# Optimization experiments

Measured on AMD Instinct MI355X. Metric: run time of the kernel, lower is better.

Reference implementation:

```python
import jax, jax.numpy as jnp
import numpy as np

NUM_FEATURE = 50


def setup_inputs() -> dict:
    key = jax.random.key(0)
    k1, k2 = jax.random.split(key)
    query = jax.random.normal(k1, (512, NUM_FEATURE), dtype=jnp.float32)
    doc = jax.random.normal(k2, (512, 256, NUM_FEATURE), dtype=jnp.float32)
    # nn.Linear(150, 1, bias=False) with weight filled with 1
    W = jnp.ones((3 * NUM_FEATURE,), dtype=jnp.float32)
    return {"query": query, "doc": doc, "W": W}


def reference(query, doc, W):
    # Split the single 150-dim linear weight into the three trilinear parts:
    # score(x, y) = w1.sen_x + w2.q_y + w3.(sen_x * q_y)
    w1, w2, w3 = W[:NUM_FEATURE], W[NUM_FEATURE:2 * NUM_FEATURE], W[2 * NUM_FEATURE:]
    q_term = query @ w2                      # [Lq]
    qw3 = query * w3                         # [Lq, d]

    def per_sentence(sen):                   # sen: [Ls, d]
        sXY = (sen @ w1)[:, None] + q_term[None, :] + sen @ qw3.T   # [Ls, Lq]
        sD2Q = jax.nn.softmax(sXY, axis=0)   # softmax over sentence tokens
        sQ2D = jax.nn.softmax(sXY, axis=1)   # softmax over query tokens
        aD2Q = sD2Q @ query                  # [Ls, d]
        aQ2D = sD2Q @ (sQ2D.T @ sen)         # (sD2Q @ sQ2D.T) @ sen, cheaper order
        return jnp.concatenate([sen, aD2Q, sen * aD2Q, sen * aQ2D], axis=1)  # [Ls, 4d]

    return jax.vmap(per_sentence)(doc)       # [n_sen, Ls, 4d]
```

## Files before the change

### kernel.cpp

```cpp
#include <hip/hip_runtime.h>
#include <math.h>

typedef __bf16 bf16_t;
typedef bf16_t bf16x2 __attribute__((ext_vector_type(2)));
typedef bf16_t bf16x4 __attribute__((ext_vector_type(4)));
typedef bf16_t bf16x8 __attribute__((ext_vector_type(8)));
typedef float f32x4 __attribute__((ext_vector_type(4)));

#define MFMA16(a,b,c) __builtin_amdgcn_mfma_f32_16x16x32_bf16((a),(b),(c),0,0,0)

#define ND 256
#define NQ 512
#define NF 50
#define L2E 1.44269504f
#define SHIFT 64.0f

#define SENT_E 0
#define PQ_E   16896
#define PD_E   33792
#define QW3_E  52224
#define QTT_E  61440
#define GT_E   70656
#define PART_B  150528
#define STATS_B 154624
#define LDS_BYTES 157952

#define ST_QTERM 0
#define ST_CI    512
#define ST_RINV  576

__launch_bounds__(1024, 4)
__global__ void ca12_kernel(const float* __restrict__ query,
                            const float* __restrict__ doc,
                            const float* __restrict__ W,
                            float* __restrict__ out)
{
    extern __shared__ char smem[];
    bf16_t* lb = (bf16_t*)smem;
    float* part  = (float*)(smem + PART_B);
    float* stats = (float*)(smem + STATS_B);

    const int tid = threadIdx.x;
    const int w = tid >> 6, l = tid & 63, ln = l & 15, lg = l >> 4;
    const int s = blockIdx.x;
    const float* sen_g = doc + (size_t)s * (ND * NF);

    auto stageQW3 = [&](int jt, int buf, int tbase, int tn) {
        const int j0 = jt * 64;
        bf16_t* dst = lb + QW3_E + buf * 4608;
        for (int e = tid - tbase; e < 1664; e += tn) {
            int jj = e / 26, c = e - jj * 26;
            if (c < 25) {
                float2 v = ((const float2*)query)[(j0 + jj) * 25 + c];
                bf16x2 p;
                p[0] = (bf16_t)(v.x * W[100 + 2 * c] * L2E);
                p[1] = (bf16_t)(v.y * W[100 + 2 * c + 1] * L2E);
                *(bf16x2*)&dst[jj * 72 + 2 * c] = p;
            } else {
                bf16x2 p;
                p[0] = (bf16_t)(stats[ST_QTERM + j0 + jj] * L2E);
                p[1] = (bf16_t)L2E;
                *(bf16x2*)&dst[jj * 72 + 50] = p;
            }
        }
    };
    auto stageQTT = [&](int jt, int buf, int tbase, int tn) {
        const int j0 = jt * 64;
        bf16_t* dst = lb + QTT_E + buf * 4608;
        for (int e = tid - tbase; e < 1600; e += tn) {
            int c = e >> 6, jj = e & 63;
            float2 v = ((const float2*)query)[(j0 + jj) * 25 + c];
            dst[(2 * c) * 72 + jj]     = (bf16_t)v.x;
            dst[(2 * c + 1) * 72 + jj] = (bf16_t)v.y;
        }
    };

    for (int e = tid; e < 924; e += 1024) {
        int f = 50 + e / 66, c4 = (e - (e / 66) * 66) * 4;
        *(bf16x4*)&lb[SENT_E + f * 264 + c4] = (bf16x4){(bf16_t)0.f,(bf16_t)0.f,(bf16_t)0.f,(bf16_t)0.f};
    }
    for (int e = tid; e < 768; e += 1024) {
        int i = e / 3, c4 = 52 + (e - (e / 3) * 3) * 4;
        *(bf16x4*)&lb[PD_E + i * 72 + c4] = (bf16x4){(bf16_t)0.f,(bf16_t)0.f,(bf16_t)0.f,(bf16_t)0.f};
    }
    for (int e = tid; e < 384; e += 1024) {
        int b = e / 192, r = e - b * 192;
        int jj = r / 3, c4 = 52 + (r - (r / 3) * 3) * 4;
        *(bf16x4*)&lb[QW3_E + b * 4608 + jj * 72 + c4] = (bf16x4){(bf16_t)0.f,(bf16_t)0.f,(bf16_t)0.f,(bf16_t)0.f};
    }
    for (int e = tid; e < 504; e += 1024) {
        int b = e / 252, r = e - b * 252;
        int f = 50 + r / 18, c4 = (r - (r / 18) * 18) * 4;
        *(bf16x4*)&lb[QTT_E + b * 4608 + f * 72 + c4] = (bf16x4){(bf16_t)0.f,(bf16_t)0.f,(bf16_t)0.f,(bf16_t)0.f};
    }
    for (int e = tid; e < 256 * 25; e += 1024) {
        int i = e / 25, c = e - i * 25;
        float2 v = ((const float2*)sen_g)[i * 25 + c];
        bf16x2 p; p[0] = (bf16_t)v.x; p[1] = (bf16_t)v.y;
        *(bf16x2*)&lb[PD_E + i * 72 + 2 * c] = p;
        lb[SENT_E + (2 * c) * 264 + i]     = p[0];
        lb[SENT_E + (2 * c + 1) * 264 + i] = p[1];
    }
    if (tid < NQ) {
        float acc = 0.f;
        #pragma unroll
        for (int c = 0; c < 25; ++c) {
            float2 v = ((const float2*)query)[tid * 25 + c];
            acc += v.x * W[NF + 2 * c] + v.y * W[NF + 2 * c + 1];
        }
        stats[ST_QTERM + tid] = acc;
    }
    if (tid < ND) {
        float acc = 0.f;
        #pragma unroll
        for (int f = 0; f < NF; ++f) acc += sen_g[tid * NF + f] * W[f];
        lb[PD_E + tid * 72 + 50] = (bf16_t)1.0f;
        lb[PD_E + tid * 72 + 51] = (bf16_t)acc;
    }
    __syncthreads();

    bf16x8 aS[2];
    #pragma unroll
    for (int ks = 0; ks < 2; ++ks)
        aS[ks] = *(bf16x8*)&lb[PD_E + (w * 16 + ln) * 72 + lg * 8 + ks * 32];
    stageQW3(0, 0, 0, 1024);
    __syncthreads();

    float rpart[4] = {0.f, 0.f, 0.f, 0.f};
    for (int jt = 0; jt < 8; ++jt) {
        if (jt < 7) stageQW3(jt + 1, (jt + 1) & 1, 0, 1024);
        const bf16_t* qb = lb + QW3_E + (jt & 1) * 4608;
        f32x4 sacc[4];
        #pragma unroll
        for (int nf = 0; nf < 4; ++nf) sacc[nf] = (f32x4){-SHIFT, -SHIFT, -SHIFT, -SHIFT};
        #pragma unroll
        for (int ks = 0; ks < 2; ++ks)
            #pragma unroll
            for (int nf = 0; nf < 4; ++nf) {
                bf16x8 b = *(bf16x8*)&qb[(nf * 16 + ln) * 72 + lg * 8 + ks * 32];
                sacc[nf] = MFMA16(aS[ks], b, sacc[nf]);
            }
        #pragma unroll
        for (int nf = 0; nf < 4; ++nf)
            #pragma unroll
            for (int r = 0; r < 4; ++r) rpart[r] += exp2f(sacc[nf][r]);
        __syncthreads();
    }
    #pragma unroll
    for (int r = 0; r < 4; ++r) {
        float v = rpart[r];
        v += __shfl_xor(v, 1);
        v += __shfl_xor(v, 2);
        v += __shfl_xor(v, 4);
        v += __shfl_xor(v, 8);
        if (ln == 0) stats[ST_RINV + w * 16 + lg * 4 + r] = 1.f / v;
    }
    __syncthreads();
    {
        const int i = tid & 255, fg = tid >> 8;
        const float rv = stats[ST_RINV + i];
        for (int f = fg; f < 50; f += 4)
            lb[SENT_E + f * 264 + i] = (bf16_t)((float)lb[SENT_E + f * 264 + i] * rv);
    }
    stageQW3(0, 0, 0, 1024);
    stageQTT(0, 0, 0, 1024);
    __syncthreads();

    f32x4 accD[4], accQ[4];
    #pragma unroll
    for (int nf = 0; nf < 4; ++nf) {
        accD[nf] = (f32x4){0.f, 0.f, 0.f, 0.f};
        accQ[nf] = (f32x4){0.f, 0.f, 0.f, 0.f};
    }
    const int mw = w & 3, nw = w >> 2;

    for (int jt = 0; jt < 8; ++jt) {
        const bf16_t* qb = lb + QW3_E + (jt & 1) * 4608;
        const bf16_t* qt = lb + QTT_E + (jt & 1) * 4608;

        f32x4 sacc[4];
        #pragma unroll
        for (int nf = 0; nf < 4; ++nf) sacc[nf] = (f32x4){-SHIFT, -SHIFT, -SHIFT, -SHIFT};
        #pragma unroll
        for (int ks = 0; ks < 2; ++ks)
            #pragma unroll
            for (int nf = 0; nf < 4; ++nf) {
                bf16x8 b = *(bf16x8*)&qb[(nf * 16 + ln) * 72 + lg * 8 + ks * 32];
                sacc[nf] = MFMA16(aS[ks], b, sacc[nf]);
            }
        #pragma unroll
        for (int nf = 0; nf < 4; ++nf) {
            #pragma unroll
            for (int r = 0; r < 4; ++r) sacc[nf][r] = exp2f(sacc[nf][r]);
            float cp = (sacc[nf][0] + sacc[nf][1]) + (sacc[nf][2] + sacc[nf][3]);
            cp += __shfl_xor(cp, 16);
            cp += __shfl_xor(cp, 32);
            if (lg == 0) part[w * 64 + nf * 16 + ln] = cp;
            bf16x4 pk;
            #pragma unroll
            for (int r = 0; r < 4; ++r) pk[r] = (bf16_t)sacc[nf][r];
            *(bf16x4*)&lb[PQ_E + (nf * 16 + ln) * 264 + w * 16 + lg * 4] = pk;
            #pragma unroll
            for (int r = 0; r < 4; ++r)
                lb[PD_E + (w * 16 + lg * 4 + r) * 72 + nf * 16 + ln] = pk[r];
        }
        __syncthreads();

        if (w == 0) {
            float cs = 0.f;
            #pragma unroll
            for (int ww = 0; ww < 16; ++ww) cs += part[ww * 64 + l];
            stats[ST_CI + l] = 1.f / cs;
        } else if (jt < 7) {
            stageQW3(jt + 1, (jt + 1) & 1, 64, 960);
            stageQTT(jt + 1, (jt + 1) & 1, 64, 960);
        }
        __syncthreads();

        bf16x8 aPs[2];
        #pragma unroll
        for (int ks = 0; ks < 2; ++ks) {
            bf16x8 raw = *(bf16x8*)&lb[PD_E + (w * 16 + ln) * 72 + lg * 8 + ks * 32];
            float4 c0 = *(const float4*)&stats[ST_CI + lg * 8 + ks * 32];
            float4 c1 = *(const float4*)&stats[ST_CI + lg * 8 + ks * 32 + 4];
            aPs[ks][0] = (bf16_t)((float)raw[0] * c0.x);
            aPs[ks][1] = (bf16_t)((float)raw[1] * c0.y);
            aPs[ks][2] = (bf16_t)((float)raw[2] * c0.z);
            aPs[ks][3] = (bf16_t)((float)raw[3] * c0.w);
            aPs[ks][4] = (bf16_t)((float)raw[4] * c1.x);
            aPs[ks][5] = (bf16_t)((float)raw[5] * c1.y);
            aPs[ks][6] = (bf16_t)((float)raw[6] * c1.z);
            aPs[ks][7] = (bf16_t)((float)raw[7] * c1.w);
        }
        #pragma unroll
        for (int ks = 0; ks < 2; ++ks)
            #pragma unroll
            for (int nf = 0; nf < 4; ++nf) {
                bf16x8 bq = *(bf16x8*)&qt[(nf * 16 + ln) * 72 + lg * 8 + ks * 32];
                accD[nf] = MFMA16(aPs[ks], bq, accD[nf]);
            }
        {
            f32x4 g = (f32x4){0.f, 0.f, 0.f, 0.f};
            #pragma unroll
            for (int ks = 0; ks < 8; ++ks) {
                bf16x8 a = *(bf16x8*)&lb[PQ_E + (mw * 16 + ln) * 264 + lg * 8 + ks * 32];
                bf16x8 b = *(bf16x8*)&lb[SENT_E + (nw * 16 + ln) * 264 + lg * 8 + ks * 32];
                g = MFMA16(a, b, g);
            }
            bf16x4 gk;
            #pragma unroll
            for (int r = 0; r < 4; ++r) gk[r] = (bf16_t)g[r];
            *(bf16x4*)&lb[GT_E + (nw * 16 + ln) * 72 + mw * 16 + lg * 4] = gk;
        }
        __syncthreads();

        #pragma unroll
        for (int ks = 0; ks < 2; ++ks)
            #pragma unroll
            for (int nf = 0; nf < 4; ++nf) {
                bf16x8 bg = *(bf16x8*)&lb[GT_E + (nf * 16 + ln) * 72 + lg * 8 + ks * 32];
                accQ[nf] = MFMA16(aPs[ks], bg, accQ[nf]);
            }
    }
    __syncthreads();

    float* ea = (float*)smem;
    float* eb = (float*)(smem + 69632);
    #pragma unroll
    for (int nf = 0; nf < 4; ++nf)
        #pragma unroll
        for (int r = 0; r < 4; ++r) {
            ea[(w * 16 + lg * 4 + r) * 68 + nf * 16 + ln] = accD[nf][r];
            eb[(w * 16 + lg * 4 + r) * 68 + nf * 16 + ln] = accQ[nf][r];
        }
    __syncthreads();
    const size_t ob0 = (size_t)s * (ND * 200);
    #pragma unroll
    for (int seg = 0; seg < 4; ++seg) {
        for (int v = tid; v < 6400; v += 1024) {
            int i = v / 25, c = v - (v / 25) * 25;
            int f = 2 * c;
            float2 o;
            if (seg == 0) {
                o = *(const float2*)&sen_g[i * 50 + f];
            } else if (seg == 1) {
                o.x = ea[i * 68 + f]; o.y = ea[i * 68 + f + 1];
            } else if (seg == 2) {
                float2 d = *(const float2*)&sen_g[i * 50 + f];
                o.x = d.x * ea[i * 68 + f]; o.y = d.y * ea[i * 68 + f + 1];
            } else {
                float2 d = *(const float2*)&sen_g[i * 50 + f];
                o.x = d.x * eb[i * 68 + f]; o.y = d.y * eb[i * 68 + f + 1];
            }
            *(float2*)&out[ob0 + (size_t)i * 200 + seg * 50 + f] = o;
        }
    }
}

extern "C" void kernel_launch(void* const* d_in, const int* in_sizes, int n_in,
                              void* d_out, int out_size, void* d_ws, size_t ws_size,
                              hipStream_t stream) {
    const float* query = (const float*)d_in[0];
    const float* doc   = (const float*)d_in[1];
    const float* W     = (const float*)d_in[2];
    float* out = (float*)d_out;
    (void)d_ws; (void)ws_size; (void)n_in; (void)in_sizes; (void)out_size;

    hipFuncSetAttribute((const void*)ca12_kernel,
                        hipFuncAttributeMaxDynamicSharedMemorySize,
                        LDS_BYTES);
    ca12_kernel<<<dim3(512), dim3(1024), LDS_BYTES, stream>>>(query, doc, W, out);
}
```

Before: 156.0 us.

## Halve block size and LDS footprint, give each wave two row tiles

Result: faster. 147.4 us (-5.5%).

```diff
diff --git a/kernel.cpp b/kernel.cpp
--- a/kernel.cpp
+++ b/kernel.cpp
@@ -16,39 +16,40 @@
 #define SHIFT 64.0f
 
 #define SENT_E 0
-#define PQ_E   16896
-#define PD_E   33792
-#define QW3_E  52224
-#define QTT_E  61440
-#define GT_E   70656
-#define PART_B  150528
-#define STATS_B 154624
-#define LDS_BYTES 157952
-
-#define ST_QTERM 0
-#define ST_CI    512
-#define ST_RINV  576
-
-__launch_bounds__(1024, 4)
-__global__ void ca12_kernel(const float* __restrict__ query,
+#define PD_E   13728
+#define PQ_E   23968
+#define QW3_E  32416
+#define QTT_E  34720
+#define GT_E   36800
+#define SEN72_E 13728
+#define P1Q_E  13728
+#define PART_B 77760
+#define QTB_B  78784
+#define RINV_B 79808
+#define LDS_BYTES 80832
+
+__launch_bounds__(512, 4)
+__global__ void ca15_kernel(const float* __restrict__ query,
                             const float* __restrict__ doc,
                             const float* __restrict__ W,
                             float* __restrict__ out)
 {
     extern __shared__ char smem[];
     bf16_t* lb = (bf16_t*)smem;
-    float* part  = (float*)(smem + PART_B);
-    float* stats = (float*)(smem + STATS_B);
+    float*  part  = (float*)(smem + PART_B);
+    bf16_t* qtb   = (bf16_t*)(smem + QTB_B);
+    float*  rinvf = (float*)(smem + RINV_B);
 
     const int tid = threadIdx.x;
     const int w = tid >> 6, l = tid & 63, ln = l & 15, lg = l >> 4;
     const int s = blockIdx.x;
     const float* sen_g = doc + (size_t)s * (ND * NF);
-
-    auto stageQW3 = [&](int jt, int buf, int tbase, int tn) {
+    const bf16x4 z4 = (bf16x4){(bf16_t)0.f,(bf16_t)0.f,(bf16_t)0.f,(bf16_t)0.f};
+
+    auto stage_p1 = [&](int jt, int buf) {
         const int j0 = jt * 64;
-        bf16_t* dst = lb + QW3_E + buf * 4608;
-        for (int e = tid - tbase; e < 1664; e += tn) {
+        bf16_t* dst = lb + P1Q_E + buf * 4608;
+        for (int e = tid; e < 1664; e += 512) {
             int jj = e / 26, c = e - jj * 26;
             if (c < 25) {
                 float2 v = ((const float2*)query)[(j0 + jj) * 25 + c];
@@ -58,242 +59,308 @@
                 *(bf16x2*)&dst[jj * 72 + 2 * c] = p;
             } else {
                 bf16x2 p;
-                p[0] = (bf16_t)(stats[ST_QTERM + j0 + jj] * L2E);
+                p[0] = (bf16_t)((float)qtb[j0 + jj] * L2E);
                 p[1] = (bf16_t)L2E;
                 *(bf16x2*)&dst[jj * 72 + 50] = p;
             }
         }
     };
-    auto stageQTT = [&](int jt, int buf, int tbase, int tn) {
-        const int j0 = jt * 64;
-        bf16_t* dst = lb + QTT_E + buf * 4608;
-        for (int e = tid - tbase; e < 1600; e += tn) {
-            int c = e >> 6, jj = e & 63;
+    auto stage_qw3 = [&](int jt) {
+        const int j0 = jt * 32;
+        bf16_t* dst = lb + QW3_E;
+        for (int e = tid; e < 832; e += 512) {
+            int jj = e / 26, c = e - jj * 26;
+            if (c < 25) {
+                float2 v = ((const float2*)query)[(j0 + jj) * 25 + c];
+                bf16x2 p;
+                p[0] = (bf16_t)(v.x * W[100 + 2 * c] * L2E);
+                p[1] = (bf16_t)(v.y * W[100 + 2 * c + 1] * L2E);
+                *(bf16x2*)&dst[jj * 72 + 2 * c] = p;
+            } else {
+                bf16x2 p;
+                p[0] = (bf16_t)((float)qtb[j0 + jj] * L2E);
+                p[1] = (bf16_t)L2E;
+                *(bf16x2*)&dst[jj * 72 + 50] = p;
+            }
+        }
+    };
+    auto stage_qtt = [&](int jt) {
+        const int j0 = jt * 32;
+        for (int e = tid; e < 800; e += 512) {
+            int c = e >> 5, jj = e & 31;
             float2 v = ((const float2*)query)[(j0 + jj) * 25 + c];
-            dst[(2 * c) * 72 + jj]     = (bf16_t)v.x;
-            dst[(2 * c + 1) * 72 + jj] = (bf16_t)v.y;
+            lb[QTT_E + (2 * c) * 40 + jj]     = (bf16_t)v.x;
+            lb[QTT_E + (2 * c + 1) * 40 + jj] = (bf16_t)v.y;
         }
     };
 
-    for (int e = tid; e < 924; e += 1024) {
+    for (int e = tid; e < 132; e += 512) {
         int f = 50 + e / 66, c4 = (e - (e / 66) * 66) * 4;
-        *(bf16x4*)&lb[SENT_E + f * 264 + c4] = (bf16x4){(bf16_t)0.f,(bf16_t)0.f,(bf16_t)0.f,(bf16_t)0.f};
-    }
-    for (int e = tid; e < 768; e += 1024) {
+        *(bf16x4*)&lb[SENT_E + f * 264 + c4] = z4;
+    }
+    for (int e = tid; e < 768; e += 512) {
         int i = e / 3, c4 = 52 + (e - (e / 3) * 3) * 4;
-        *(bf16x4*)&lb[PD_E + i * 72 + c4] = (bf16x4){(bf16_t)0.f,(bf16_t)0.f,(bf16_t)0.f,(bf16_t)0.f};
-    }
-    for (int e = tid; e < 384; e += 1024) {
-        int b = e / 192, r = e - b * 192;
-        int jj = r / 3, c4 = 52 + (r - (r / 3) * 3) * 4;
-        *(bf16x4*)&lb[QW3_E + b * 4608 + jj * 72 + c4] = (bf16x4){(bf16_t)0.f,(bf16_t)0.f,(bf16_t)0.f,(bf16_t)0.f};
-    }
-    for (int e = tid; e < 504; e += 1024) {
-        int b = e / 252, r = e - b * 252;
-        int f = 50 + r / 18, c4 = (r - (r / 18) * 18) * 4;
-        *(bf16x4*)&lb[QTT_E + b * 4608 + f * 72 + c4] = (bf16x4){(bf16_t)0.f,(bf16_t)0.f,(bf16_t)0.f,(bf16_t)0.f};
-    }
-    for (int e = tid; e < 256 * 25; e += 1024) {
-        int i = e / 25, c = e - i * 25;
+        *(bf16x4*)&lb[SEN72_E + i * 72 + c4] = z4;
+    }
+    for (int e = tid; e < 6400; e += 512) {
+        int i = e / 25, c = e - (e / 25) * 25;
         float2 v = ((const float2*)sen_g)[i * 25 + c];
         bf16x2 p; p[0] = (bf16_t)v.x; p[1] = (bf16_t)v.y;
-        *(bf16x2*)&lb[PD_E + i * 72 + 2 * c] = p;
+        *(bf16x2*)&lb[SEN72_E + i * 72 + 2 * c] = p;
         lb[SENT_E + (2 * c) * 264 + i]     = p[0];
         lb[SENT_E + (2 * c + 1) * 264 + i] = p[1];
     }
-    if (tid < NQ) {
+    {
         float acc = 0.f;
         #pragma unroll
         for (int c = 0; c < 25; ++c) {
             float2 v = ((const float2*)query)[tid * 25 + c];
             acc += v.x * W[NF + 2 * c] + v.y * W[NF + 2 * c + 1];
         }
-        stats[ST_QTERM + tid] = acc;
+        qtb[tid] = (bf16_t)acc;
     }
     if (tid < ND) {
         float acc = 0.f;
         #pragma unroll
-        for (int f = 0; f < NF; ++f) acc += sen_g[tid * NF + f] * W[f];
-        lb[PD_E + tid * 72 + 50] = (bf16_t)1.0f;
-        lb[PD_E + tid * 72 + 51] = (bf16_t)acc;
-    }
-    __syncthreads();
-
-    bf16x8 aS[2];
-    #pragma unroll
-    for (int ks = 0; ks < 2; ++ks)
-        aS[ks] = *(bf16x8*)&lb[PD_E + (w * 16 + ln) * 72 + lg * 8 + ks * 32];
-    stageQW3(0, 0, 0, 1024);
-    __syncthreads();
-
-    float rpart[4] = {0.f, 0.f, 0.f, 0.f};
+        for (int c = 0; c < 25; ++c) {
+            float2 v = ((const float2*)sen_g)[tid * 25 + c];
+            acc += v.x * W[2 * c] + v.y * W[2 * c + 1];
+        }
+        lb[SEN72_E + tid * 72 + 50] = (bf16_t)1.0f;
+        lb[SEN72_E + tid * 72 + 51] = (bf16_t)acc;
+    }
+    __syncthreads();
+
+    bf16x8 aS[2][2];
+    #pragma unroll
+    for (int mf = 0; mf < 2; ++mf)
+        #pragma unroll
+        for (int ks = 0; ks < 2; ++ks)
+            aS[mf][ks] = *(bf16x8*)&lb[SEN72_E + (w * 32 + mf * 16 + ln) * 72 + lg * 8 + ks * 32];
+    __syncthreads();
+
+    for (int e = tid; e < 384; e += 512) {
+        int buf = e / 192, r = e - buf * 192;
+        int jj = r / 3, c4 = 52 + (r - (r / 3) * 3) * 4;
+        *(bf16x4*)&lb[P1Q_E + buf * 4608 + jj * 72 + c4] = z4;
+    }
+    stage_p1(0, 0);
+    __syncthreads();
+
+    float rpart[2][4] = {{0.f,0.f,0.f,0.f},{0.f,0.f,0.f,0.f}};
     for (int jt = 0; jt < 8; ++jt) {
-        if (jt < 7) stageQW3(jt + 1, (jt + 1) & 1, 0, 1024);
-        const bf16_t* qb = lb + QW3_E + (jt & 1) * 4608;
-        f32x4 sacc[4];
-        #pragma unroll
-        for (int nf = 0; nf < 4; ++nf) sacc[nf] = (f32x4){-SHIFT, -SHIFT, -SHIFT, -SHIFT};
+        if (jt < 7) stage_p1(jt + 1, (jt + 1) & 1);
+        const bf16_t* qb = lb + P1Q_E + (jt & 1) * 4608;
+        f32x4 sacc[2][4];
+        #pragma unroll
+        for (int mf = 0; mf < 2; ++mf)
+            #pragma unroll
+            for (int nf = 0; nf < 4; ++nf)
+                sacc[mf][nf] = (f32x4){-SHIFT, -SHIFT, -SHIFT, -SHIFT};
         #pragma unroll
         for (int ks = 0; ks < 2; ++ks)
             #pragma unroll
             for (int nf = 0; nf < 4; ++nf) {
                 bf16x8 b = *(bf16x8*)&qb[(nf * 16 + ln) * 72 + lg * 8 + ks * 32];
-                sacc[nf] = MFMA16(aS[ks], b, sacc[nf]);
-            }
-        #pragma unroll
-        for (int nf = 0; nf < 4; ++nf)
-            #pragma unroll
-            for (int r = 0; r < 4; ++r) rpart[r] += exp2f(sacc[nf][r]);
+                sacc[0][nf] = MFMA16(aS[0][ks], b, sacc[0][nf]);
+                sacc[1][nf] = MFMA16(aS[1][ks], b, sacc[1][nf]);
+            }
+        #pragma unroll
+        for (int mf = 0; mf < 2; ++mf)
+            #pragma unroll
+            for (int nf = 0; nf < 4; ++nf)
+                #pragma unroll
+                for (int r = 0; r < 4; ++r)
+                    rpart[mf][r] += exp2f(sacc[mf][nf][r]);
         __syncthreads();
     }
     #pragma unroll
-    for (int r = 0; r < 4; ++r) {
-        float v = rpart[r];
-        v += __shfl_xor(v, 1);
-        v += __shfl_xor(v, 2);
-        v += __shfl_xor(v, 4);
-        v += __shfl_xor(v, 8);
-        if (ln == 0) stats[ST_RINV + w * 16 + lg * 4 + r] = 1.f / v;
-    }
-    __syncthreads();
-    {
-        const int i = tid & 255, fg = tid >> 8;
-        const float rv = stats[ST_RINV + i];
-        for (int f = fg; f < 50; f += 4)
-            lb[SENT_E + f * 264 + i] = (bf16_t)((float)lb[SENT_E + f * 264 + i] * rv);
-    }
-    stageQW3(0, 0, 0, 1024);
-    stageQTT(0, 0, 0, 1024);
-    __syncthreads();
-
-    f32x4 accD[4], accQ[4];
+    for (int mf = 0; mf < 2; ++mf)
+        #pragma unroll
+        for (int r = 0; r < 4; ++r) {
+            float v = rpart[mf][r];
+            v += __shfl_xor(v, 1);
+            v += __shfl_xor(v, 2);
+            v += __shfl_xor(v, 4);
+            v += __shfl_xor(v, 8);
+            if (ln == 0) rinvf[w * 32 + mf * 16 + lg * 4 + r] = 1.f / v;
+        }
+    __syncthreads();
+    for (int e = tid; e < 12800; e += 512) {
+        int f = e / 256, i = e & 255;
+        lb[SENT_E + f * 264 + i] = (bf16_t)((float)lb[SENT_E + f * 264 + i] * rinvf[i]);
+    }
+    for (int e = tid; e < 96; e += 512) {
+        int jj = e / 3, c4 = 52 + (e - (e / 3) * 3) * 4;
+        *(bf16x4*)&lb[QW3_E + jj * 72 + c4] = z4;
+    }
+    stage_qw3(0);
+    __syncthreads();
+
+    f32x4 accD[2][4], accQ[2][4];
+    #pragma unroll
+    for (int mf = 0; mf < 2; ++mf)
+        #pragma unroll
+        for (int nf = 0; nf < 4; ++nf) {
+            accD[mf][nf] = (f32x4){0.f, 0.f, 0.f, 0.f};
+            accQ[mf][nf] = (f32x4){0.f, 0.f, 0.f, 0.f};
+        }
+    bf16x8 aPs[2];
+    const int jf = w & 1, ff = w >> 1;
+    int qtt_row[4], gt_row[4];
     #pragma unroll
     for (int nf = 0; nf < 4; ++nf) {
-        accD[nf] = (f32x4){0.f, 0.f, 0.f, 0.f};
-        accQ[nf] = (f32x4){0.f, 0.f, 0.f, 0.f};
-    }
-    const int mw = w & 3, nw = w >> 2;
-
-    for (int jt = 0; jt < 8; ++jt) {
-        const bf16_t* qb = lb + QW3_E + (jt & 1) * 4608;
-        const bf16_t* qt = lb + QTT_E + (jt & 1) * 4608;
-
-        f32x4 sacc[4];
-        #pragma unroll
-        for (int nf = 0; nf < 4; ++nf) sacc[nf] = (f32x4){-SHIFT, -SHIFT, -SHIFT, -SHIFT};
+        int f = nf * 16 + ln;
+        int rc = f < 51 ? f : 51;
+        qtt_row[nf] = QTT_E + rc * 40;
+        gt_row[nf]  = GT_E + rc * 40;
+    }
+    const int fg = ff * 16 + ln;
+    const int sent_row = SENT_E + (fg < 51 ? fg : 51) * 264;
+
+    for (int jt = 0; jt < 16; ++jt) {
+        if (jt > 0) {
+            #pragma unroll
+            for (int nf = 0; nf < 4; ++nf) {
+                bf16x8 bg = *(bf16x8*)&lb[gt_row[nf] + lg * 8];
+                accQ[0][nf] = MFMA16(aPs[0], bg, accQ[0][nf]);
+                accQ[1][nf] = MFMA16(aPs[1], bg, accQ[1][nf]);
+            }
+        }
+        f32x4 sacc[2][2];
+        #pragma unroll
+        for (int mf = 0; mf < 2; ++mf)
+            #pragma unroll
+            for (int n2 = 0; n2 < 2; ++n2)
+                sacc[mf][n2] = (f32x4){-SHIFT, -SHIFT, -SHIFT, -SHIFT};
         #pragma unroll
         for (int ks = 0; ks < 2; ++ks)
             #pragma unroll
-            for (int nf = 0; nf < 4; ++nf) {
-                bf16x8 b = *(bf16x8*)&qb[(nf * 16 + ln) * 72 + lg * 8 + ks * 32];
-                sacc[nf] = MFMA16(aS[ks], b, sacc[nf]);
-            }
-        #pragma unroll
-        for (int nf = 0; nf < 4; ++nf) {
-            #pragma unroll
-            for (int r = 0; r < 4; ++r) sacc[nf][r] = exp2f(sacc[nf][r]);
-            float cp = (sacc[nf][0] + sacc[nf][1]) + (sacc[nf][2] + sacc[nf][3]);
+            for (int n2 = 0; n2 < 2; ++n2) {
+                bf16x8 b = *(bf16x8*)&lb[QW3_E + (n2 * 16 + ln) * 72 + lg * 8 + ks * 32];
+                sacc[0][n2] = MFMA16(aS[0][ks], b, sacc[0][n2]);
+                sacc[1][n2] = MFMA16(aS[1][ks], b, sacc[1][n2]);
+            }
+        #pragma unroll
+        for (int n2 = 0; n2 < 2; ++n2) {
+            #pragma unroll
+            for (int mf = 0; mf < 2; ++mf)
+                #pragma unroll
+                for (int r = 0; r < 4; ++r)
+                    sacc[mf][n2][r] = exp2f(sacc[mf][n2][r]);
+            float cp = ((sacc[0][n2][0] + sacc[0][n2][1]) + (sacc[0][n2][2] + sacc[0][n2][3]))
+                     + ((sacc[1][n2][0] + sacc[1][n2][1]) + (sacc[1][n2][2] + sacc[1][n2][3]));
             cp += __shfl_xor(cp, 16);
             cp += __shfl_xor(cp, 32);
-            if (lg == 0) part[w * 64 + nf * 16 + ln] = cp;
-            bf16x4 pk;
-            #pragma unroll
-            for (int r = 0; r < 4; ++r) pk[r] = (bf16_t)sacc[nf][r];
-            *(bf16x4*)&lb[PQ_E + (nf * 16 + ln) * 264 + w * 16 + lg * 4] = pk;
-            #pragma unroll
-            for (int r = 0; r < 4; ++r)
-                lb[PD_E + (w * 16 + lg * 4 + r) * 72 + nf * 16 + ln] = pk[r];
-        }
+            if (lg == 0) part[w * 32 + n2 * 16 + ln] = cp;
+            #pragma unroll
+            for (int mf = 0; mf < 2; ++mf) {
+                bf16x4 pk;
+                #pragma unroll
+                for (int r = 0; r < 4; ++r) pk[r] = (bf16_t)sacc[mf][n2][r];
+                *(bf16x4*)&lb[PQ_E + (n2 * 16 + ln) * 264 + w * 32 + mf * 16 + lg * 4] = pk;
+                #pragma unroll
+                for (int r = 0; r < 4; ++r)
+                    lb[PD_E + (w * 32 + mf * 16 + lg * 4 + r) * 40 + n2 * 16 + ln] = pk[r];
+            }
+        }
+        stage_qtt(jt);
         __syncthreads();
 
-        if (w == 0) {
-            float cs = 0.f;
-            #pragma unroll
-            for (int ww = 0; ww < 16; ++ww) cs += part[ww * 64 + l];
-            stats[ST_CI + l] = 1.f / cs;
-        } else if (jt < 7) {
-            stageQW3(jt + 1, (jt + 1) & 1, 64, 960);
-            stageQTT(jt + 1, (jt + 1) & 1, 64, 960);
-        }
-        __syncthreads();
-
-        bf16x8 aPs[2];
-        #pragma unroll
-        for (int ks = 0; ks < 2; ++ks) {
-            bf16x8 raw = *(bf16x8*)&lb[PD_E + (w * 16 + ln) * 72 + lg * 8 + ks * 32];
-            float4 c0 = *(const float4*)&stats[ST_CI + lg * 8 + ks * 32];
-            float4 c1 = *(const float4*)&stats[ST_CI + lg * 8 + ks * 32 + 4];
-            aPs[ks][0] = (bf16_t)((float)raw[0] * c0.x);
-            aPs[ks][1] = (bf16_t)((float)raw[1] * c0.y);
-            aPs[ks][2] = (bf16_t)((float)raw[2] * c0.z);
-            aPs[ks][3] = (bf16_t)((float)raw[3] * c0.w);
-            aPs[ks][4] = (bf16_t)((float)raw[4] * c1.x);
-            aPs[ks][5] = (bf16_t)((float)raw[5] * c1.y);
-            aPs[ks][6] = (bf16_t)((float)raw[6] * c1.z);
-            aPs[ks][7] = (bf16_t)((float)raw[7] * c1.w);
-        }
-        #pragma unroll
-        for (int ks = 0; ks < 2; ++ks)
-            #pragma unroll
-            for (int nf = 0; nf < 4; ++nf) {
-                bf16x8 bq = *(bf16x8*)&qt[(nf * 16 + ln) * 72 + lg * 8 + ks * 32];
-                accD[nf] = MFMA16(aPs[ks], bq, accD[nf]);
-            }
+        float cs = 0.f;
+        #pragma unroll
+        for (int ww = 0; ww < 8; ++ww) cs += part[ww * 32 + (l & 31)];
+        float civ = 1.f / cs;
+        float cv[8];
+        #pragma unroll
+        for (int e = 0; e < 8; ++e) cv[e] = __shfl(civ, lg * 8 + e);
+        #pragma unroll
+        for (int mf = 0; mf < 2; ++mf) {
+            bf16x8 raw = *(bf16x8*)&lb[PD_E + (w * 32 + mf * 16 + ln) * 40 + lg * 8];
+            #pragma unroll
+            for (int e = 0; e < 8; ++e)
+                aPs[mf][e] = (bf16_t)((float)raw[e] * cv[e]);
+        }
+        #pragma unroll
+        for (int nf = 0; nf < 4; ++nf) {
+            bf16x8 bq = *(bf16x8*)&lb[qtt_row[nf] + lg * 8];
+            accD[0][nf] = MFMA16(aPs[0], bq, accD[0][nf]);
+            accD[1][nf] = MFMA16(aPs[1], bq, accD[1][nf]);
+        }
         {
             f32x4 g = (f32x4){0.f, 0.f, 0.f, 0.f};
             #pragma unroll
             for (int ks = 0; ks < 8; ++ks) {
-                bf16x8 a = *(bf16x8*)&lb[PQ_E + (mw * 16 + ln) * 264 + lg * 8 + ks * 32];
-                bf16x8 b = *(bf16x8*)&lb[SENT_E + (nw * 16 + ln) * 264 + lg * 8 + ks * 32];
+                bf16x8 a = *(bf16x8*)&lb[PQ_E + (jf * 16 + ln) * 264 + ks * 32 + lg * 8];
+                bf16x8 b = *(bf16x8*)&lb[sent_row + ks * 32 + lg * 8];
                 g = MFMA16(a, b, g);
             }
-            bf16x4 gk;
-            #pragma unroll
-            for (int r = 0; r < 4; ++r) gk[r] = (bf16_t)g[r];
-            *(bf16x4*)&lb[GT_E + (nw * 16 + ln) * 72 + mw * 16 + lg * 4] = gk;
-        }
+            if (fg < 52) {
+                bf16x4 gk;
+                #pragma unroll
+                for (int r = 0; r < 4; ++r) gk[r] = (bf16_t)g[r];
+                *(bf16x4*)&lb[GT_E + fg * 40 + jf * 16 + lg * 4] = gk;
+            }
+        }
+        if (jt < 15) stage_qw3(jt + 1);
         __syncthreads();
-
-        #pragma unroll
-        for (int ks = 0; ks < 2; ++ks)
-            #pragma unroll
-            for (int nf = 0; nf < 4; ++nf) {
-                bf16x8 bg = *(bf16x8*)&lb[GT_E + (nf * 16 + ln) * 72 + lg * 8 + ks * 32];
-                accQ[nf] = MFMA16(aPs[ks], bg, accQ[nf]);
-            }
+    }
+    #pragma unroll
+    for (int nf = 0; nf < 4; ++nf) {
+        bf16x8 bg = *(bf16x8*)&lb[gt_row[nf] + lg * 8];
+        accQ[0][nf] = MFMA16(aPs[0], bg, accQ[0][nf]);
+        accQ[1][nf] = MFMA16(aPs[1], bg, accQ[1][nf]);
     }
     __syncthreads();
 
     float* ea = (float*)smem;
-    float* eb = (float*)(smem + 69632);
-    #pragma unroll
-    for (int nf = 0; nf < 4; ++nf)
-        #pragma unroll
-        for (int r = 0; r < 4; ++r) {
-            ea[(w * 16 + lg * 4 + r) * 68 + nf * 16 + ln] = accD[nf][r];
-            eb[(w * 16 + lg * 4 + r) * 68 + nf * 16 + ln] = accQ[nf][r];
+    #pragma unroll
+    for (int mf = 0; mf < 2; ++mf)
+        #pragma unroll
+        for (int nf = 0; nf < 4; ++nf) {
+            int f = nf * 16 + ln;
+            if (f < 56)
+                #pragma unroll
+                for (int r = 0; r < 4; ++r)
+                    ea[(w * 32 + mf * 16 + lg * 4 + r) * 56 + f] = accD[mf][nf][r];
         }
     __syncthreads();
     const size_t ob0 = (size_t)s * (ND * 200);
-    #pragma unroll
-    for (int seg = 0; seg < 4; ++seg) {
-        for (int v = tid; v < 6400; v += 1024) {
-            int i = v / 25, c = v - (v / 25) * 25;
-            int f = 2 * c;
-            float2 o;
-            if (seg == 0) {
-                o = *(const float2*)&sen_g[i * 50 + f];
-            } else if (seg == 1) {
-                o.x = ea[i * 68 + f]; o.y = ea[i * 68 + f + 1];
-            } else if (seg == 2) {
-                float2 d = *(const float2*)&sen_g[i * 50 + f];
-                o.x = d.x * ea[i * 68 + f]; o.y = d.y * ea[i * 68 + f + 1];
-            } else {
-                float2 d = *(const float2*)&sen_g[i * 50 + f];
-                o.x = d.x * eb[i * 68 + f]; o.y = d.y * eb[i * 68 + f + 1];
-            }
-            *(float2*)&out[ob0 + (size_t)i * 200 + seg * 50 + f] = o;
-        }
+    for (int v = tid; v < 6400; v += 512) {
+        int i = v / 25, c = v - (v / 25) * 25, f = 2 * c;
+        *(float2*)&out[ob0 + (size_t)i * 200 + f] = *(const float2*)&sen_g[i * 50 + f];
+    }
+    for (int v = tid; v < 6400; v += 512) {
+        int i = v / 25, c = v - (v / 25) * 25, f = 2 * c;
+        float2 o;
+        o.x = ea[i * 56 + f]; o.y = ea[i * 56 + f + 1];
+        *(float2*)&out[ob0 + (size_t)i * 200 + 50 + f] = o;
+    }
+    for (int v = tid; v < 6400; v += 512) {
+        int i = v / 25, c = v - (v / 25) * 25, f = 2 * c;
+        float2 d = *(const float2*)&sen_g[i * 50 + f];
+        float2 o;
+        o.x = d.x * ea[i * 56 + f]; o.y = d.y * ea[i * 56 + f + 1];
+        *(float2*)&out[ob0 + (size_t)i * 200 + 100 + f] = o;
+    }
+    __syncthreads();
+    #pragma unroll
+    for (int mf = 0; mf < 2; ++mf)
+        #pragma unroll
+        for (int nf = 0; nf < 4; ++nf) {
+            int f = nf * 16 + ln;
+            if (f < 56)
+                #pragma unroll
+                for (int r = 0; r < 4; ++r)
+                    ea[(w * 32 + mf * 16 + lg * 4 + r) * 56 + f] = accQ[mf][nf][r];
+        }
+    __syncthreads();
+    for (int v = tid; v < 6400; v += 512) {
+        int i = v / 25, c = v - (v / 25) * 25, f = 2 * c;
+        float2 d = *(const float2*)&sen_g[i * 50 + f];
+        float2 o;
+        o.x = d.x * ea[i * 56 + f]; o.y = d.y * ea[i * 56 + f + 1];
+        *(float2*)&out[ob0 + (size_t)i * 200 + 150 + f] = o;
     }
 }
 
@@ -306,8 +373,8 @@
     float* out = (float*)d_out;
     (void)d_ws; (void)ws_size; (void)n_in; (void)in_sizes; (void)out_size;
 
-    hipFuncSetAttribute((const void*)ca12_kernel,
+    hipFuncSetAttribute((const void*)ca15_kernel,
                         hipFuncAttributeMaxDynamicSharedMemorySize,
                         LDS_BYTES);
-    ca12_kernel<<<dim3(512), dim3(1024), LDS_BYTES, stream>>>(query, doc, W, out);
+    ca15_kernel<<<dim3(512), dim3(512), LDS_BYTES, stream>>>(query, doc, W, out);
 }
```
